# Performance work log

Measured on AMD Instinct MI355X. Metric: run time of the kernel, lower is better.

Reference implementation:

```python
import jax, jax.numpy as jnp
import numpy as np

N_FEATURES = 1_000_000
N_FIELDS = 50
EMB_DIM = 64
ATT_DIM = EMB_DIM // 2
BATCH = 2048


def setup_inputs() -> dict:
    key = jax.random.key(0)
    ks = jax.random.split(key, 7)
    features = jax.random.randint(ks[0], (BATCH, N_FIELDS), 0, N_FEATURES)
    emb_table = jax.random.normal(ks[1], (N_FEATURES, EMB_DIM), dtype=jnp.float32) * 0.01
    coeff_table = jax.random.normal(ks[2], (N_FEATURES, 1), dtype=jnp.float32) * 0.01
    bias = jnp.zeros((1,), dtype=jnp.float32)
    # kaiming normal for relu: std = sqrt(2/fan_in)
    att_w = jax.random.normal(ks[3], (ATT_DIM, EMB_DIM), dtype=jnp.float32) * np.sqrt(2.0 / EMB_DIM)
    att_b = jnp.zeros((ATT_DIM,), dtype=jnp.float32)
    p = jax.random.normal(ks[4], (ATT_DIM, 1), dtype=jnp.float32)
    w = jnp.ones((EMB_DIM, 1), dtype=jnp.float32)
    return {"features": features, "emb_table": emb_table, "coeff_table": coeff_table,
            "bias": bias, "att_w": att_w, "att_b": att_b, "p": p, "w": w}


def reference(features, emb_table, coeff_table, bias, att_w, att_b, p, w):
    # Dropout layers in eval mode (identity).
    emb = emb_table[features]            # [B, F, D]
    coeff = coeff_table[features]        # [B, F, 1]
    iu, ju = jnp.triu_indices(N_FIELDS, k=1)
    # pairwise hadamard products in row-major (i,j) order matching the loop
    interactions = emb[:, iu, :] * emb[:, ju, :]   # [B, P, D], P = F*(F-1)/2
    # attention MLP: relu(x @ att_w^T + att_b) @ p -> scores over interactions
    hidden = jax.nn.relu(jnp.einsum('bpd,ad->bpa', interactions, att_w) + att_b)
    scores = jnp.einsum('bpa,ao->bpo', hidden, p)  # [B, P, 1]
    att = jax.nn.softmax(scores, axis=1)           # softmax over interaction dim
    pooled = jnp.sum(interactions * att, axis=1)   # [B, D]
    interaction_part = (pooled @ w).reshape(-1)    # [B]
    linear_part = jnp.sum(coeff, axis=1).reshape(-1)
    return interaction_part + linear_part + bias
```

## Files before the change

kernel.cpp:

```cpp
#include <hip/hip_runtime.h>
#include <hip/hip_fp16.h>
#include <math.h>

#define NFIELDS 50
#define EMBD 64
#define NPAIRS 1225
#define NTILEPAD 40
#define NPAD (NTILEPAD * 32)
#define NELEM 2
#define NWPE 2
#define NITER2 20
#define NTHREADS 256
#define NFPAD 51
#define CHSTR (NFPAD * 8)

typedef _Float16 f16x8 __attribute__((ext_vector_type(8)));
typedef _Float16 f16x2 __attribute__((ext_vector_type(2)));
typedef __fp16   fp16x2 __attribute__((ext_vector_type(2)));
typedef float f32x16 __attribute__((ext_vector_type(16)));

union F16x8U { f16x8 v; f16x2 h2[4]; unsigned int u[4]; uint4 q; };
union U32F { unsigned int u; f16x2 h; fp16x2 g; };

__device__ __forceinline__ f16x2 pkrtz(float a, float b) {
    U32F t; t.g = __builtin_amdgcn_cvt_pkrtz(a, b);
    return t.h;
}

__device__ __forceinline__ f16x2 pkmax0(f16x2 a) {
#if __has_builtin(__builtin_elementwise_max)
    f16x2 z; z[0] = (_Float16)0; z[1] = (_Float16)0;
    return __builtin_elementwise_max(a, z);
#else
    f16x2 r;
    r[0] = a[0] > (_Float16)0 ? a[0] : (_Float16)0;
    r[1] = a[1] > (_Float16)0 ? a[1] : (_Float16)0;
    return r;
#endif
}

__launch_bounds__(NTHREADS, 4)
__global__ void afm_kernel(const int* __restrict__ features,
                           const float* __restrict__ emb_table,
                           const float* __restrict__ coeff_table,
                           const float* __restrict__ bias,
                           const float* __restrict__ att_w,
                           const float* __restrict__ att_b,
                           const float* __restrict__ pvec,
                           const float* __restrict__ wvec,
                           float* __restrict__ out)
{
    __shared__ __align__(16) unsigned short emb3[NELEM][8][NFPAD][8];
    __shared__ unsigned short pair_s[NPAD];
    __shared__ int   feat_s[NELEM][NFIELDS];
    __shared__ float red_s[NELEM][NWPE], red_st[NELEM][NWPE];
    __shared__ float red_c[NELEM];

    const int b0   = blockIdx.x * NELEM;
    const int tid  = threadIdx.x;
    const int lane = tid & 63;
    const int wid  = tid >> 6;
    const int col  = lane & 31;
    const int h    = lane >> 5;
    const int h4   = h * 4;

    const int eh = tid >> 7;
    const int tl = tid & 127;
    int myfeat = 0;
    if (tl < NFIELDS) {
        myfeat = features[(b0 + eh) * NFIELDS + tl];
        feat_s[eh][tl] = myfeat;
    }
    #pragma unroll
    for (int k = 0; k < NPAD / NTHREADS; ++k) {
        const int q = tid + k * NTHREADS;
        int i = 0, j = 1;
        if (q < NPAIRS) {
            const float s = sqrtf((float)(9801 - 8 * q));
            i = (int)((99.0f - s) * 0.5f);
            const int off = i * NFIELDS - ((i * (i + 1)) >> 1);
            j = i + 1 + (q - off);
        }
        pair_s[q] = (unsigned short)((i << 8) | j);
    }
    if ((wid & 1) == 0) {
        float cacc = 0.f;
        if (lane < NFIELDS)       cacc = coeff_table[myfeat];
        else if (lane == NFIELDS) cacc = bias[0];
        #pragma unroll
        for (int m = 1; m < 64; m <<= 1) cacc += __shfl_xor(cacc, m, 64);
        if (lane == 0) red_c[wid >> 1] = cacc;
    }

    f16x8 afragW[4];
    f16x2 w2[16];
    #pragma unroll
    for (int c = 0; c < 4; ++c) {
        const int d0 = c * 16 + h * 8;
        const float4 wa0 = *reinterpret_cast<const float4*>(&att_w[col * EMBD + d0]);
        const float4 wa1 = *reinterpret_cast<const float4*>(&att_w[col * EMBD + d0 + 4]);
        F16x8U bf;
        bf.v[0] = (_Float16)wa0.x; bf.v[1] = (_Float16)wa0.y;
        bf.v[2] = (_Float16)wa0.z; bf.v[3] = (_Float16)wa0.w;
        bf.v[4] = (_Float16)wa1.x; bf.v[5] = (_Float16)wa1.y;
        bf.v[6] = (_Float16)wa1.z; bf.v[7] = (_Float16)wa1.w;
        afragW[c] = bf.v;
        const float4 wv0 = *reinterpret_cast<const float4*>(&wvec[d0]);
        const float4 wv1 = *reinterpret_cast<const float4*>(&wvec[d0 + 4]);
        f16x2 t0; t0[0] = (_Float16)wv0.x; t0[1] = (_Float16)wv0.y; w2[c * 4 + 0] = t0;
        f16x2 t1; t1[0] = (_Float16)wv0.z; t1[1] = (_Float16)wv0.w; w2[c * 4 + 1] = t1;
        f16x2 t2; t2[0] = (_Float16)wv1.x; t2[1] = (_Float16)wv1.y; w2[c * 4 + 2] = t2;
        f16x2 t3; t3[0] = (_Float16)wv1.z; t3[1] = (_Float16)wv1.w; w2[c * 4 + 3] = t3;
    }
    float attb_r[16];
    f16x2 p16[8];
    #pragma unroll
    for (int q = 0; q < 4; ++q) {
        const float4 ab = *reinterpret_cast<const float4*>(&att_b[8 * q + 4 * h]);
        attb_r[4 * q + 0] = ab.x; attb_r[4 * q + 1] = ab.y;
        attb_r[4 * q + 2] = ab.z; attb_r[4 * q + 3] = ab.w;
        const float4 pp = *reinterpret_cast<const float4*>(&pvec[8 * q + 4 * h]);
        f16x2 pa; pa[0] = (_Float16)pp.x; pa[1] = (_Float16)pp.y; p16[2 * q]     = pa;
        f16x2 pb; pb[0] = (_Float16)pp.z; pb[1] = (_Float16)pp.w; p16[2 * q + 1] = pb;
    }
    __syncthreads();

    #pragma unroll
    for (int k = 0; k < 7; ++k) {
        const int idx = tid + k * NTHREADS;
        if (idx < NELEM * NFIELDS * 16) {
            const int e  = idx >= NFIELDS * 16;
            const int r  = idx - e * NFIELDS * 16;
            const int f  = r >> 4;
            const int d0 = (r & 15) * 4;
            const float4 v = *reinterpret_cast<const float4*>(
                &emb_table[(size_t)feat_s[e][f] * EMBD + d0]);
            const int c  = d0 >> 4;
            const int hh = (d0 >> 3) & 1;
            const int e0 = d0 & 7;
            U32F t0, t1;
            t0.h[0] = (_Float16)v.x; t0.h[1] = (_Float16)v.y;
            t1.h[0] = (_Float16)v.z; t1.h[1] = (_Float16)v.w;
            uint2 pk; pk.x = t0.u; pk.y = t1.u;
            *reinterpret_cast<uint2*>(&emb3[e][hh * 4 + c][f][e0]) = pk;
        }
    }
    __syncthreads();

    const int ee = wid >> 1;
    const int wv = wid & 1;
    const unsigned short* const ebase = &emb3[ee][0][0][0] + h4 * CHSTR;
    float s_run = 0.f, st_run = 0.f;

    #pragma unroll 2
    for (int tt = 0; tt < NITER2; ++tt) {
        const int tile = wv + tt * NWPE;
        const int q    = tile * 32 + col;
        const unsigned int ij = pair_s[q];
        const int fi = ij >> 8;
        const int fj = ij & 255;

        const unsigned short* pi = ebase + fi * 8;
        const unsigned short* pj = ebase + fj * 8;

        f32x16 acc;
        #pragma unroll
        for (int reg = 0; reg < 16; ++reg) acc[reg] = attb_r[reg];

        f16x2 th2; th2[0] = (_Float16)0; th2[1] = (_Float16)0;
        #pragma unroll
        for (int c = 0; c < 4; ++c) {
            F16x8U ai, aj;
            ai.q = *reinterpret_cast<const uint4*>(pi + c * CHSTR);
            aj.q = *reinterpret_cast<const uint4*>(pj + c * CHSTR);
            const f16x2 x0 = ai.h2[0] * aj.h2[0];
            const f16x2 x1 = ai.h2[1] * aj.h2[1];
            const f16x2 x2 = ai.h2[2] * aj.h2[2];
            const f16x2 x3 = ai.h2[3] * aj.h2[3];
            th2 = x0 * w2[c * 4 + 0] + th2;
            th2 = x1 * w2[c * 4 + 1] + th2;
            th2 = x2 * w2[c * 4 + 2] + th2;
            th2 = x3 * w2[c * 4 + 3] + th2;
            F16x8U bf;
            bf.h2[0] = x0; bf.h2[1] = x1; bf.h2[2] = x2; bf.h2[3] = x3;
            acc = __builtin_amdgcn_mfma_f32_32x32x16_f16(afragW[c], bf.v, acc, 0, 0, 0);
        }

        f16x2 sp2; sp2[0] = (_Float16)0; sp2[1] = (_Float16)0;
        #pragma unroll
        for (int qq = 0; qq < 8; ++qq) {
            const f16x2 av = pkmax0(pkrtz(acc[2 * qq], acc[2 * qq + 1]));
            sp2 = av * p16[qq] + sp2;
        }
        const float sp     = (float)sp2[0] + (float)sp2[1];
        const float t_half = (float)th2[0] + (float)th2[1];

        U32F pkd, oth;
        pkd.h = pkrtz(sp, t_half);
        oth.u = (unsigned int)__shfl_xor((int)pkd.u, 32, 64);
        const float sc = sp + (float)oth.h[0];
        const float tf = t_half + (float)oth.h[1];

        const float e = (q < NPAIRS) ? __expf(sc) : 0.f;
        s_run  += e;
        st_run += e * tf;
    }

    #pragma unroll
    for (int m = 1; m < 64; m <<= 1) {
        s_run  += __shfl_xor(s_run, m, 64);
        st_run += __shfl_xor(st_run, m, 64);
    }
    if (lane == 0) { red_s[ee][wv] = s_run; red_st[ee][wv] = st_run; }
    __syncthreads();

    if (tl == 0) {
        const float S  = red_s[eh][0] + red_s[eh][1];
        const float ST = red_st[eh][0] + red_st[eh][1];
        out[b0 + eh] = ST / S + red_c[eh];
    }
}

extern "C" void kernel_launch(void* const* d_in, const int* in_sizes, int n_in,
                              void* d_out, int out_size, void* d_ws, size_t ws_size,
                              hipStream_t stream) {
    const int*   features    = (const int*)d_in[0];
    const float* emb_table   = (const float*)d_in[1];
    const float* coeff_table = (const float*)d_in[2];
    const float* bias        = (const float*)d_in[3];
    const float* att_w       = (const float*)d_in[4];
    const float* att_b       = (const float*)d_in[5];
    const float* pvec        = (const float*)d_in[6];
    const float* wvec        = (const float*)d_in[7];
    float* out = (float*)d_out;

    const int batch = in_sizes[0] / NFIELDS;
    afm_kernel<<<batch / NELEM, NTHREADS, 0, stream>>>(
        features, emb_table, coeff_table, bias, att_w, att_b, pvec, wvec, out);
}
```

Before: 32.73 us.

## Process four batch elements per block with double-buffered embedding prefetch

Each block now handles four batch elements one after another instead of two at once, and all four waves share the pair tiles of one element. The embedding gather for the next element goes into registers while the current element is computed, then is written to the other LDS buffer, so gather latency overlaps compute. Per-block setup (pair table, weight fragments) is amortized over more elements. In exchange the grid is halved to 512 blocks, launch bounds drop to 3 blocks per SM, and a barrier is added per element, which may reduce parallelism across the GPU.

Result: faster. 29.81 us (-8.9%).

```diff
diff --git a/kernel.cpp b/kernel.cpp
--- a/kernel.cpp
+++ b/kernel.cpp
@@ -7,9 +7,9 @@
 #define NPAIRS 1225
 #define NTILEPAD 40
 #define NPAD (NTILEPAD * 32)
-#define NELEM 2
-#define NWPE 2
-#define NITER2 20
+#define NSEQ 4
+#define NWAVES 4
+#define NITER 10
 #define NTHREADS 256
 #define NFPAD 51
 #define CHSTR (NFPAD * 8)
@@ -39,7 +39,7 @@
 #endif
 }
 
-__launch_bounds__(NTHREADS, 4)
+__launch_bounds__(NTHREADS, 3)
 __global__ void afm_kernel(const int* __restrict__ features,
                            const float* __restrict__ emb_table,
                            const float* __restrict__ coeff_table,
@@ -50,13 +50,13 @@
                            const float* __restrict__ wvec,
                            float* __restrict__ out)
 {
-    __shared__ __align__(16) unsigned short emb3[NELEM][8][NFPAD][8];
+    __shared__ __align__(16) unsigned short emb3[2][8][NFPAD][8];
     __shared__ unsigned short pair_s[NPAD];
-    __shared__ int   feat_s[NELEM][NFIELDS];
-    __shared__ float red_s[NELEM][NWPE], red_st[NELEM][NWPE];
-    __shared__ float red_c[NELEM];
-
-    const int b0   = blockIdx.x * NELEM;
+    __shared__ int   feat_s[NSEQ][NFIELDS];
+    __shared__ float red_s[2][NWAVES], red_st[2][NWAVES];
+    __shared__ float csum_s[NSEQ];
+
+    const int b0   = blockIdx.x * NSEQ;
     const int tid  = threadIdx.x;
     const int lane = tid & 63;
     const int wid  = tid >> 6;
@@ -64,13 +64,20 @@
     const int h    = lane >> 5;
     const int h4   = h * 4;
 
-    const int eh = tid >> 7;
-    const int tl = tid & 127;
-    int myfeat = 0;
-    if (tl < NFIELDS) {
-        myfeat = features[(b0 + eh) * NFIELDS + tl];
-        feat_s[eh][tl] = myfeat;
-    }
+    {
+        float cacc = 0.f;
+        if (lane < NFIELDS) {
+            const int f = features[(b0 + wid) * NFIELDS + lane];
+            feat_s[wid][lane] = f;
+            cacc = coeff_table[f];
+        } else if (lane == NFIELDS) {
+            cacc = bias[0];
+        }
+        #pragma unroll
+        for (int m = 1; m < 64; m <<= 1) cacc += __shfl_xor(cacc, m, 64);
+        if (lane == 0) csum_s[wid] = cacc;
+    }
+
     #pragma unroll
     for (int k = 0; k < NPAD / NTHREADS; ++k) {
         const int q = tid + k * NTHREADS;
@@ -82,14 +89,6 @@
             j = i + 1 + (q - off);
         }
         pair_s[q] = (unsigned short)((i << 8) | j);
-    }
-    if ((wid & 1) == 0) {
-        float cacc = 0.f;
-        if (lane < NFIELDS)       cacc = coeff_table[myfeat];
-        else if (lane == NFIELDS) cacc = bias[0];
-        #pragma unroll
-        for (int m = 1; m < 64; m <<= 1) cacc += __shfl_xor(cacc, m, 64);
-        if (lane == 0) red_c[wid >> 1] = cacc;
     }
 
     f16x8 afragW[4];
@@ -125,100 +124,129 @@
     }
     __syncthreads();
 
-    #pragma unroll
-    for (int k = 0; k < 7; ++k) {
-        const int idx = tid + k * NTHREADS;
-        if (idx < NELEM * NFIELDS * 16) {
-            const int e  = idx >= NFIELDS * 16;
-            const int r  = idx - e * NFIELDS * 16;
-            const int f  = r >> 4;
-            const int d0 = (r & 15) * 4;
-            const float4 v = *reinterpret_cast<const float4*>(
-                &emb_table[(size_t)feat_s[e][f] * EMBD + d0]);
-            const int c  = d0 >> 4;
-            const int hh = (d0 >> 3) & 1;
-            const int e0 = d0 & 7;
-            U32F t0, t1;
-            t0.h[0] = (_Float16)v.x; t0.h[1] = (_Float16)v.y;
-            t1.h[0] = (_Float16)v.z; t1.h[1] = (_Float16)v.w;
-            uint2 pk; pk.x = t0.u; pk.y = t1.u;
-            *reinterpret_cast<uint2*>(&emb3[e][hh * 4 + c][f][e0]) = pk;
-        }
-    }
+    float4 greg[4];
+
+#define GISSUE(ee)                                                          \
+    {                                                                       \
+        _Pragma("unroll")                                                   \
+        for (int k = 0; k < 4; ++k) {                                       \
+            const int idx = tid + k * NTHREADS;                             \
+            if (idx < NFIELDS * 16) {                                       \
+                const int f  = idx >> 4;                                    \
+                const int d0 = (idx & 15) * 4;                              \
+                greg[k] = *reinterpret_cast<const float4*>(                 \
+                    &emb_table[(size_t)feat_s[ee][f] * EMBD + d0]);         \
+            }                                                               \
+        }                                                                   \
+    }
+
+#define GWRITE(buf)                                                         \
+    {                                                                       \
+        _Pragma("unroll")                                                   \
+        for (int k = 0; k < 4; ++k) {                                       \
+            const int idx = tid + k * NTHREADS;                             \
+            if (idx < NFIELDS * 16) {                                       \
+                const int f  = idx >> 4;                                    \
+                const int d0 = (idx & 15) * 4;                              \
+                const int c  = d0 >> 4;                                     \
+                const int hh = (d0 >> 3) & 1;                               \
+                const int e0 = d0 & 7;                                      \
+                U32F t0, t1;                                                \
+                t0.h[0] = (_Float16)greg[k].x; t0.h[1] = (_Float16)greg[k].y; \
+                t1.h[0] = (_Float16)greg[k].z; t1.h[1] = (_Float16)greg[k].w; \
+                uint2 pk; pk.x = t0.u; pk.y = t1.u;                         \
+                *reinterpret_cast<uint2*>(&emb3[buf][hh * 4 + c][f][e0]) = pk; \
+            }                                                               \
+        }                                                                   \
+    }
+
+    GISSUE(0);
+    GWRITE(0);
     __syncthreads();
 
-    const int ee = wid >> 1;
-    const int wv = wid & 1;
-    const unsigned short* const ebase = &emb3[ee][0][0][0] + h4 * CHSTR;
-    float s_run = 0.f, st_run = 0.f;
-
-    #pragma unroll 2
-    for (int tt = 0; tt < NITER2; ++tt) {
-        const int tile = wv + tt * NWPE;
-        const int q    = tile * 32 + col;
-        const unsigned int ij = pair_s[q];
-        const int fi = ij >> 8;
-        const int fj = ij & 255;
-
-        const unsigned short* pi = ebase + fi * 8;
-        const unsigned short* pj = ebase + fj * 8;
-
-        f32x16 acc;
+    #pragma unroll 1
+    for (int e = 0; e < NSEQ; ++e) {
+        if (e + 1 < NSEQ) GISSUE(e + 1);
+
+        const unsigned short* const ebase =
+            &emb3[e & 1][0][0][0] + h4 * CHSTR;
+        float s_run = 0.f, st_run = 0.f;
+
+        #pragma unroll 2
+        for (int tt = 0; tt < NITER; ++tt) {
+            const int tile = wid + tt * NWAVES;
+            const int q    = tile * 32 + col;
+            const unsigned int ij = pair_s[q];
+            const int fi = ij >> 8;
+            const int fj = ij & 255;
+
+            const unsigned short* pi = ebase + fi * 8;
+            const unsigned short* pj = ebase + fj * 8;
+
+            f32x16 acc;
+            #pragma unroll
+            for (int reg = 0; reg < 16; ++reg) acc[reg] = attb_r[reg];
+
+            f16x2 th2; th2[0] = (_Float16)0; th2[1] = (_Float16)0;
+            #pragma unroll
+            for (int c = 0; c < 4; ++c) {
+                F16x8U ai, aj;
+                ai.q = *reinterpret_cast<const uint4*>(pi + c * CHSTR);
+                aj.q = *reinterpret_cast<const uint4*>(pj + c * CHSTR);
+                const f16x2 x0 = ai.h2[0] * aj.h2[0];
+                const f16x2 x1 = ai.h2[1] * aj.h2[1];
+                const f16x2 x2 = ai.h2[2] * aj.h2[2];
+                const f16x2 x3 = ai.h2[3] * aj.h2[3];
+                th2 = x0 * w2[c * 4 + 0] + th2;
+                th2 = x1 * w2[c * 4 + 1] + th2;
+                th2 = x2 * w2[c * 4 + 2] + th2;
+                th2 = x3 * w2[c * 4 + 3] + th2;
+                F16x8U bf;
+                bf.h2[0] = x0; bf.h2[1] = x1; bf.h2[2] = x2; bf.h2[3] = x3;
+                acc = __builtin_amdgcn_mfma_f32_32x32x16_f16(afragW[c], bf.v, acc, 0, 0, 0);
+            }
+
+            f16x2 sp2; sp2[0] = (_Float16)0; sp2[1] = (_Float16)0;
+            #pragma unroll
+            for (int qq = 0; qq < 8; ++qq) {
+                const f16x2 av = pkmax0(pkrtz(acc[2 * qq], acc[2 * qq + 1]));
+                sp2 = av * p16[qq] + sp2;
+            }
+            const float sp     = (float)sp2[0] + (float)sp2[1];
+            const float t_half = (float)th2[0] + (float)th2[1];
+
+            U32F pkd, oth;
+            pkd.h = pkrtz(sp, t_half);
+            oth.u = (unsigned int)__shfl_xor((int)pkd.u, 32, 64);
+            const float sc = sp + (float)oth.h[0];
+            const float tf = t_half + (float)oth.h[1];
+
+            const float ex = (q < NPAIRS) ? __expf(sc) : 0.f;
+            s_run  += ex;
+            st_run += ex * tf;
+        }
+
         #pragma unroll
-        for (int reg = 0; reg < 16; ++reg) acc[reg] = attb_r[reg];
-
-        f16x2 th2; th2[0] = (_Float16)0; th2[1] = (_Float16)0;
-        #pragma unroll
-        for (int c = 0; c < 4; ++c) {
-            F16x8U ai, aj;
-            ai.q = *reinterpret_cast<const uint4*>(pi + c * CHSTR);
-            aj.q = *reinterpret_cast<const uint4*>(pj + c * CHSTR);
-            const f16x2 x0 = ai.h2[0] * aj.h2[0];
-            const f16x2 x1 = ai.h2[1] * aj.h2[1];
-            const f16x2 x2 = ai.h2[2] * aj.h2[2];
-            const f16x2 x3 = ai.h2[3] * aj.h2[3];
-            th2 = x0 * w2[c * 4 + 0] + th2;
-            th2 = x1 * w2[c * 4 + 1] + th2;
-            th2 = x2 * w2[c * 4 + 2] + th2;
-            th2 = x3 * w2[c * 4 + 3] + th2;
-            F16x8U bf;
-            bf.h2[0] = x0; bf.h2[1] = x1; bf.h2[2] = x2; bf.h2[3] = x3;
-            acc = __builtin_amdgcn_mfma_f32_32x32x16_f16(afragW[c], bf.v, acc, 0, 0, 0);
-        }
-
-        f16x2 sp2; sp2[0] = (_Float16)0; sp2[1] = (_Float16)0;
-        #pragma unroll
-        for (int qq = 0; qq < 8; ++qq) {
-            const f16x2 av = pkmax0(pkrtz(acc[2 * qq], acc[2 * qq + 1]));
-            sp2 = av * p16[qq] + sp2;
-        }
-        const float sp     = (float)sp2[0] + (float)sp2[1];
-        const float t_half = (float)th2[0] + (float)th2[1];
-
-        U32F pkd, oth;
-        pkd.h = pkrtz(sp, t_half);
-        oth.u = (unsigned int)__shfl_xor((int)pkd.u, 32, 64);
-        const float sc = sp + (float)oth.h[0];
-        const float tf = t_half + (float)oth.h[1];
-
-        const float e = (q < NPAIRS) ? __expf(sc) : 0.f;
-        s_run  += e;
-        st_run += e * tf;
-    }
-
-    #pragma unroll
-    for (int m = 1; m < 64; m <<= 1) {
-        s_run  += __shfl_xor(s_run, m, 64);
-        st_run += __shfl_xor(st_run, m, 64);
-    }
-    if (lane == 0) { red_s[ee][wv] = s_run; red_st[ee][wv] = st_run; }
-    __syncthreads();
-
-    if (tl == 0) {
-        const float S  = red_s[eh][0] + red_s[eh][1];
-        const float ST = red_st[eh][0] + red_st[eh][1];
-        out[b0 + eh] = ST / S + red_c[eh];
-    }
+        for (int m = 1; m < 64; m <<= 1) {
+            s_run  += __shfl_xor(s_run, m, 64);
+            st_run += __shfl_xor(st_run, m, 64);
+        }
+        if (lane == 0) { red_s[e & 1][wid] = s_run; red_st[e & 1][wid] = st_run; }
+
+        if (e + 1 < NSEQ) GWRITE((e + 1) & 1);
+        __syncthreads();
+
+        if (tid == 0) {
+            const float S  = red_s[e & 1][0] + red_s[e & 1][1]
+                           + red_s[e & 1][2] + red_s[e & 1][3];
+            const float ST = red_st[e & 1][0] + red_st[e & 1][1]
+                           + red_st[e & 1][2] + red_st[e & 1][3];
+            out[b0 + e] = ST / S + csum_s[e];
+        }
+    }
+
+#undef GISSUE
+#undef GWRITE
 }
 
 extern "C" void kernel_launch(void* const* d_in, const int* in_sizes, int n_in,
@@ -235,6 +263,6 @@
     float* out = (float*)d_out;
 
     const int batch = in_sizes[0] / NFIELDS;
-    afm_kernel<<<batch / NELEM, NTHREADS, 0, stream>>>(
+    afm_kernel<<<batch / NSEQ, NTHREADS, 0, stream>>>(
         features, emb_table, coeff_table, bias, att_w, att_b, pvec, wvec, out);
 }
```
